# Kernel optimization log

Hardware: AMD Instinct MI355X
Metric: run time of the kernel (lower is better)

Reference implementation:

```python
import jax, jax.numpy as jnp
import numpy as np

B = 65536      # batch
C = 1000       # num_classes
D = 256        # feat_dim


def _l2norm(x, eps=1e-12):
    # matches F.normalize(dim=1): v / max(||v||_2, eps)
    n = jnp.linalg.norm(x, axis=1, keepdims=True)
    return x / jnp.maximum(n, eps)


def setup_inputs() -> dict:
    key = jax.random.key(0)
    k1, k2, k3, k4, k5 = jax.random.split(key, 5)
    bound = 1.0 / np.sqrt(D)
    X = jax.random.normal(k1, (B, D), dtype=jnp.float32)
    labels = jax.random.randint(k2, (B,), 0, C)
    signatures = jax.random.uniform(k3, (C, D), dtype=jnp.float32, minval=-bound, maxval=bound)
    b_means = jax.random.uniform(k4, (1, D), dtype=jnp.float32, minval=-bound, maxval=bound)
    b_covs = jax.random.normal(k5, (D, D), dtype=jnp.float32)
    return {"X": X, "labels": labels, "signatures": signatures,
            "b_means": b_means, "b_covs": b_covs}


def reference(X, labels, signatures, b_means, b_covs):
    # SVD-based whitening of background covariance (tiny DxD)
    cov = b_covs @ b_covs.T
    U, eig, _ = jnp.linalg.svd(cov)
    DU = (eig ** -0.5)[:, None] * U.T              # diag(eig^-1/2) @ U^T, [D, D]
    xHat = _l2norm((X - b_means) @ DU.T)           # [B, D]
    sHat = _l2norm(signatures @ DU.T)              # [C, D]
    ACE_targets = xHat @ sHat.T                    # [B, C] cosine scores
    labels = labels.astype(jnp.int32)
    numerator = jnp.take_along_axis(ACE_targets, labels[:, None], axis=1)[:, 0]
    # denominator = exp(true) + sum(exp(others)) == sum over all classes
    loss = -jnp.mean(numerator - jax.nn.logsumexp(ACE_targets, axis=1))
    return (loss, ACE_targets)
```

## Files before the change

### kernel.cpp

```cpp
#include <hip/hip_runtime.h>
#include <hip/hip_bf16.h>
#include <math.h>

#define D_ 256
#define B_ 65536
#define C_ 1000

typedef _Float16 f16x8 __attribute__((ext_vector_type(8)));
typedef _Float16 f16x4 __attribute__((ext_vector_type(4)));
typedef float f32x4 __attribute__((ext_vector_type(4)));

__global__ void transpose_kernel(const float* __restrict__ in, float* __restrict__ out,
                                 double* __restrict__ acc) {
  __shared__ float t[32][33];
  if (blockIdx.x == 0 && threadIdx.x == 0) *acc = 0.0;
  const int bx = blockIdx.x & 7, by = blockIdx.x >> 3;
  const int lx = threadIdx.x & 31, ly = threadIdx.x >> 5;
#pragma unroll
  for (int s = 0; s < 4; ++s) {
    int r = by * 32 + ly + s * 8;
    t[ly + s * 8][lx] = in[r * 256 + bx * 32 + lx];
  }
  __syncthreads();
#pragma unroll
  for (int s = 0; s < 4; ++s) {
    int r = bx * 32 + ly + s * 8;
    out[r * 256 + by * 32 + lx] = t[lx][ly + s * 8];
  }
}

__global__ void cov_kernel(const float* __restrict__ bc, const float* __restrict__ bcT,
                           double* __restrict__ C64) {
  const int i = blockIdx.x, j = threadIdx.x;
  __shared__ float ri[D_];
  ri[j] = bc[i * D_ + j];
  __syncthreads();
  double s = 0.0;
#pragma unroll 8
  for (int k = 0; k < D_; ++k) s += (double)ri[k] * (double)bcT[k * D_ + j];
  C64[i * D_ + j] = s;
}

__global__ __launch_bounds__(256, 1) void chol_panel(double* __restrict__ A, int p) {
  const int j0 = p * 64;
  const int r = threadIdx.x;
  __shared__ double rowv[64];
  __shared__ double dinv;
  double pr[64];
  const bool act = (r >= j0);
  if (act) {
#pragma unroll
    for (int k = 0; k < 64; ++k) pr[k] = A[(size_t)r * D_ + j0 + k];
  }
#pragma unroll
  for (int j = 0; j < 64; ++j) {
    const int col = j0 + j;
    if (r == col) { double d = sqrt(pr[j]); pr[j] = d; dinv = 1.0 / d; }
    __syncthreads();
    if (r > col) {
      double lr = pr[j] * dinv;
      pr[j] = lr;
      if (r < j0 + 64) rowv[r - j0] = lr;
    }
    __syncthreads();
    if (r > col) {
      const double lr = pr[j];
#pragma unroll
      for (int k = j + 1; k < 64; ++k) pr[k] -= lr * rowv[k];
    }
  }
  if (act) {
    const int kmax = (r - j0 < 63) ? (r - j0) : 63;
#pragma unroll
    for (int k = 0; k < 64; ++k)
      if (k <= kmax) A[(size_t)r * D_ + j0 + k] = pr[k];
  }
}

__global__ __launch_bounds__(256) void chol_trail(double* __restrict__ A, int p) {
  const int j0 = p * 64;
  const int t0 = j0 + 64;
  int b = blockIdx.x, I = 0;
  while (b >= I + 1) { b -= I + 1; ++I; }
  const int J = b;
  const int r0 = t0 + I * 64, c0 = t0 + J * 64;
  __shared__ double LR[64][67];
  __shared__ double LC[64][67];
  const int tid = threadIdx.x;
  for (int e = tid; e < 64 * 64; e += 256) {
    int rr = e >> 6, cc = e & 63;
    LR[rr][cc] = A[(size_t)(r0 + rr) * D_ + j0 + cc];
    LC[rr][cc] = A[(size_t)(c0 + rr) * D_ + j0 + cc];
  }
  __syncthreads();
  const int tx = tid & 15, ty = tid >> 4;
  double acc[4][4];
#pragma unroll
  for (int i = 0; i < 4; ++i)
#pragma unroll
    for (int j = 0; j < 4; ++j) acc[i][j] = 0.0;
#pragma unroll 4
  for (int k = 0; k < 64; ++k) {
    double a_[4], b_[4];
#pragma unroll
    for (int i = 0; i < 4; ++i) a_[i] = LR[ty + 16 * i][k];
#pragma unroll
    for (int j = 0; j < 4; ++j) b_[j] = LC[tx + 16 * j][k];
#pragma unroll
    for (int i = 0; i < 4; ++i)
#pragma unroll
      for (int j = 0; j < 4; ++j) acc[i][j] += a_[i] * b_[j];
  }
#pragma unroll
  for (int i = 0; i < 4; ++i) {
    const int grow = r0 + ty + 16 * i;
#pragma unroll
    for (int j = 0; j < 4; ++j) {
      const int gcol = c0 + tx + 16 * j;
      A[(size_t)grow * D_ + gcol] -= acc[i][j];
    }
  }
}

__global__ __launch_bounds__(256) void inv_kernel(const double* __restrict__ L,
                                                  _Float16* __restrict__ Wb,
                                                  _Float16* __restrict__ WbT) {
  const int c = blockIdx.x;
  const int tid = threadIdx.x;
  __shared__ double w[D_];
  __shared__ double rdi[D_];
  __shared__ double rhs[32];
  __shared__ double Ldd[32][33];
  w[tid] = 0.0;
  rdi[tid] = 1.0 / L[(size_t)tid * D_ + tid];
  __syncthreads();
  const int q0 = c >> 5;
  for (int q = q0; q < 8; ++q) {
    const int i0 = q * 32;
    const int ii = tid >> 3, s = tid & 7;
    const int i = i0 + ii;
    double part = 0.0;
    for (int k = c + s; k < i0; k += 8) part += L[(size_t)i * D_ + k] * w[k];
    part += __shfl_xor(part, 1, 64);
    part += __shfl_xor(part, 2, 64);
    part += __shfl_xor(part, 4, 64);
    if (s == 0) rhs[ii] = ((i == c) ? 1.0 : 0.0) - part;
    for (int e = tid; e < 32 * 32; e += 256) {
      int rr = e >> 5, cc = e & 31;
      Ldd[rr][cc] = L[(size_t)(i0 + rr) * D_ + i0 + cc];
    }
    __syncthreads();
    if (tid < 32) {
      double x = rhs[tid];
      double v = 0.0;
      for (int j = 0; j < 32; ++j) {
        double xj = __shfl(x, j, 64);
        double wj = xj * rdi[i0 + j];
        if (tid == j) v = wj;
        if (tid > j) x -= Ldd[tid][j] * wj;
      }
      w[i0 + tid] = v;
    }
    __syncthreads();
  }
  _Float16 h = (_Float16)(float)w[tid];
  WbT[(size_t)c * D_ + tid] = h;
  Wb[(size_t)tid * D_ + c] = h;
}

__global__ void sig_kernel(const float* __restrict__ S, const _Float16* __restrict__ WbT,
                           _Float16* __restrict__ sHatP) {
  int c = blockIdx.x, i = threadIdx.x;
  const int g = c >> 4, lr = c & 15;
  const int ks = i >> 5, lq = (i >> 3) & 3, jj = i & 7;
  const size_t off = (size_t)(g * 8 + ks) * 512 + (size_t)(lq * 16 + lr) * 8 + jj;
  if (c >= C_) { sHatP[off] = (_Float16)0.0f; return; }
  __shared__ float srow[D_];
  __shared__ float wred[4];
  srow[i] = S[c * D_ + i];
  __syncthreads();
  float t = 0.f;
  for (int k = 0; k < D_; ++k) t += (float)WbT[k * D_ + i] * srow[k];
  float ss = t * t;
#pragma unroll
  for (int d = 1; d < 64; d <<= 1) ss += __shfl_xor(ss, d, 64);
  if ((i & 63) == 0) wred[i >> 6] = ss;
  __syncthreads();
  float tot = wred[0] + wred[1] + wred[2] + wred[3];
  float rn = 1.0f / fmaxf(sqrtf(tot), 1e-12f);
  sHatP[off] = (_Float16)(t * rn);
}

__global__ __launch_bounds__(256) void xform_kernel(const float* __restrict__ X,
                                                    const float* __restrict__ means,
                                                    const _Float16* __restrict__ Wb,
                                                    _Float16* __restrict__ xHat,
                                                    float* __restrict__ rnX) {
  __shared__ __align__(16) _Float16 As[64 * D_];
  __shared__ __align__(16) _Float16 Bs[128 * D_];
  __shared__ float msh[D_];
  const int tid = threadIdx.x;
  const int rowbase = blockIdx.x * 64;
  msh[tid] = means[tid];
  __syncthreads();
  for (int s = 0; s < 16; ++s) {
    int c = s * 256 + tid;
    int r = c >> 6, q = c & 63;
    const float4 xv = *(const float4*)(X + (size_t)(rowbase + r) * D_ + q * 4);
    f16x4 hv;
    hv[0] = (_Float16)(xv.x - msh[q * 4 + 0]);
    hv[1] = (_Float16)(xv.y - msh[q * 4 + 1]);
    hv[2] = (_Float16)(xv.z - msh[q * 4 + 2]);
    hv[3] = (_Float16)(xv.w - msh[q * 4 + 3]);
    int byte = (q * 8) ^ ((r & 7) << 4);
    *(f16x4*)((char*)(As + r * D_) + byte) = hv;
  }
  const int w = tid >> 6, l = tid & 63, lr = l & 15, lq = l >> 4;
  float ss[4] = {0.f, 0.f, 0.f, 0.f};
  for (int ch = 0; ch < 2; ++ch) {
    __syncthreads();
    for (int s = 0; s < 16; ++s) {
      int c = s * 256 + tid;
      int r = c >> 5, q = c & 31;
      uint4 v = *(const uint4*)(Wb + (size_t)(ch * 128 + r) * D_ + q * 8);
      int byte = (q * 16) ^ ((r & 7) << 4);
      *(uint4*)((char*)(Bs + r * D_) + byte) = v;
    }
    __syncthreads();
    f32x4 acc[8];
#pragma unroll
    for (int t = 0; t < 8; ++t) acc[t] = (f32x4){0.f, 0.f, 0.f, 0.f};
#pragma unroll
    for (int ks = 0; ks < 8; ++ks) {
      int arow = w * 16 + lr;
      int abyte = (ks * 64 + lq * 16) ^ ((arow & 7) << 4);
      f16x8 af = *(const f16x8*)((char*)(As + arow * D_) + abyte);
#pragma unroll
      for (int t = 0; t < 8; ++t) {
        int brow = t * 16 + lr;
        int bbyte = (ks * 64 + lq * 16) ^ ((brow & 7) << 4);
        f16x8 bf = *(const f16x8*)((char*)(Bs + brow * D_) + bbyte);
        acc[t] = __builtin_amdgcn_mfma_f32_16x16x32_f16(af, bf, acc[t], 0, 0, 0);
      }
    }
#pragma unroll
    for (int t = 0; t < 8; ++t) {
      int col = ch * 128 + t * 16 + lr;
#pragma unroll
      for (int j = 0; j < 4; ++j) {
        int row = rowbase + w * 16 + lq * 4 + j;
        float v = acc[t][j];
        ss[j] += v * v;
        xHat[(size_t)row * D_ + col] = (_Float16)v;
      }
    }
  }
#pragma unroll
  for (int d = 1; d < 16; d <<= 1) {
#pragma unroll
    for (int j = 0; j < 4; ++j) ss[j] += __shfl_xor(ss[j], d, 64);
  }
  if (lr == 0) {
#pragma unroll
    for (int j = 0; j < 4; ++j) {
      int row = rowbase + w * 16 + lq * 4 + j;
      rnX[row] = 1.0f / fmaxf(sqrtf(ss[j]), 1e-12f);
    }
  }
}

__global__ __launch_bounds__(256) void ace_kernel(const _Float16* __restrict__ xHat,
                                                  const _Float16* __restrict__ sHatP,
                                                  const float* __restrict__ rnX,
                                                  const int* __restrict__ labels,
                                                  float* __restrict__ outACE,
                                                  double* __restrict__ acc_loss) {
  __shared__ float part[16];
  const int tid = threadIdx.x;
  const int w = tid >> 6, l = tid & 63, lr = l & 15, lq = l >> 4;
  const int rowbase = blockIdx.x * 64;
  const int arow = rowbase + w * 16 + lr;

  f16x8 a[8];
  {
    const _Float16* ap = xHat + (size_t)arow * D_ + lq * 8;
#pragma unroll
    for (int ks = 0; ks < 8; ++ks) a[ks] = *(const f16x8*)(ap + ks * 32);
  }

  int lab[4]; float rx[4], ssum[4], num[4];
#pragma unroll
  for (int j = 0; j < 4; ++j) {
    int row = rowbase + w * 16 + lq * 4 + j;
    lab[j] = labels[row];
    rx[j] = rnX[row];
    ssum[j] = 0.f; num[j] = 0.f;
  }

  const _Float16* bl = sHatP + (size_t)l * 8;
  float* const outrow = outACE + (size_t)(rowbase + w * 16 + lq * 4) * C_;

  for (int ch = 0; ch < 8; ++ch) {
    f32x4 acc[8];
#pragma unroll
    for (int t = 0; t < 8; ++t) acc[t] = (f32x4){0.f, 0.f, 0.f, 0.f};
#pragma unroll
    for (int ks = 0; ks < 8; ++ks) {
#pragma unroll
      for (int t = 0; t < 8; ++t) {
        f16x8 bf = *(const f16x8*)(bl + (size_t)((ch * 8 + t) * 8 + ks) * 512);
        acc[t] = __builtin_amdgcn_mfma_f32_16x16x32_f16(a[ks], bf, acc[t], 0, 0, 0);
      }
    }
#pragma unroll
    for (int t = 0; t < 8; ++t) {
      const int col = ch * 128 + t * 16 + lr;
#pragma unroll
      for (int j = 0; j < 4; ++j) {
        float v = acc[t][j] * rx[j];
        if (col < C_) outrow[(size_t)j * C_ + col] = v;
        ssum[j] += __expf(v - 1.0f);
        num[j] = (col == lab[j]) ? v : num[j];
      }
    }
  }
#pragma unroll
  for (int d2 = 1; d2 < 16; d2 <<= 1) {
#pragma unroll
    for (int j = 0; j < 4; ++j) {
      ssum[j] += __shfl_xor(ssum[j], d2, 64);
      num[j]  += __shfl_xor(num[j], d2, 64);
    }
  }
  if (lr == 0) {
    const float padcorr = 24.0f * __expf(-1.0f);
    float contrib = 0.f;
#pragma unroll
    for (int j = 0; j < 4; ++j)
      contrib += num[j] - (1.0f + __logf(ssum[j] - padcorr));
    part[w * 4 + lq] = contrib;
  }
  __syncthreads();
  if (tid == 0) {
    float s = 0.f;
#pragma unroll
    for (int p2 = 0; p2 < 16; ++p2) s += part[p2];
    atomicAdd(acc_loss, (double)s);
  }
}

__global__ void fin_kernel(const double* a, float* out) {
  out[0] = (float)(-(*a) / (double)B_);
}

extern "C" void kernel_launch(void* const* d_in, const int* in_sizes, int n_in,
                              void* d_out, int out_size, void* d_ws, size_t ws_size,
                              hipStream_t stream) {
  const float* X      = (const float*)d_in[0];
  const int*   labels = (const int*)d_in[1];
  const float* S      = (const float*)d_in[2];
  const float* means  = (const float*)d_in[3];
  const float* bc     = (const float*)d_in[4];
  float* out = (float*)d_out;

  char* w = (char*)d_ws;
  double*    acc   = (double*)(w + 0);
  double*    C64   = (double*)(w + 256);
  _Float16*  Wb    = (_Float16*)(w + 524544);
  _Float16*  WbT   = (_Float16*)(w + 655616);
  _Float16*  sHatP = (_Float16*)(w + 786688);
  float*     rnX   = (float*)(w + 1310976);
  _Float16*  xHat  = (_Float16*)(w + 1573120);
  float*     bcT   = (float*)(w + 1573120);

  transpose_kernel<<<64, 256, 0, stream>>>(bc, bcT, acc);
  cov_kernel<<<256, 256, 0, stream>>>(bc, bcT, C64);
  for (int p = 0; p < 4; ++p) {
    chol_panel<<<1, 256, 0, stream>>>(C64, p);
    int nt = 3 - p;
    if (nt > 0) chol_trail<<<nt * (nt + 1) / 2, 256, 0, stream>>>(C64, p);
  }
  inv_kernel<<<256, 256, 0, stream>>>(C64, Wb, WbT);
  sig_kernel<<<1024, 256, 0, stream>>>(S, WbT, sHatP);
  xform_kernel<<<1024, 256, 0, stream>>>(X, means, Wb, xHat, rnX);
  ace_kernel<<<1024, 256, 0, stream>>>(xHat, sHatP, rnX, labels, out + 1, acc);
  fin_kernel<<<1, 1, 0, stream>>>(acc, out);
}
```

Baseline: 446.5 us.

## Stage signature tiles into LDS with double-buffered async loads in ace kernel

The ace kernel now uses 512-thread blocks covering 128 rows and stages each 128-class chunk of the packed signature matrix into shared memory with global_load_lds, double-buffered so the next chunk loads during the current chunk's MFMAs. Before, each wave read B fragments straight from global or L2 memory. The aim is to cut redundant global traffic for the B operand by sharing it across 8 waves and to hide load latency. In exchange it uses 128KB of LDS per block, which caps occupancy at one block per CU, and adds a block barrier per chunk.

```diff
diff --git a/kernel.cpp b/kernel.cpp
--- a/kernel.cpp
+++ b/kernel.cpp
@@ -269,21 +269,22 @@
   }
 }
 
-__global__ __launch_bounds__(256) void ace_kernel(const _Float16* __restrict__ xHat,
+__global__ __launch_bounds__(512) void ace_kernel(const _Float16* __restrict__ xHat,
                                                   const _Float16* __restrict__ sHatP,
                                                   const float* __restrict__ rnX,
                                                   const int* __restrict__ labels,
                                                   float* __restrict__ outACE,
                                                   double* __restrict__ acc_loss) {
-  __shared__ float part[16];
+  __shared__ __align__(16) _Float16 Bsh[2][64 * 512];
+  __shared__ float part[32];
   const int tid = threadIdx.x;
-  const int w = tid >> 6, l = tid & 63, lr = l & 15, lq = l >> 4;
-  const int rowbase = blockIdx.x * 64;
-  const int arow = rowbase + w * 16 + lr;
+  const int wid = tid >> 6, l = tid & 63, lr = l & 15, lq = l >> 4;
+  const int rowbase = blockIdx.x * 128;
+  const int wrow = rowbase + wid * 16;
 
   f16x8 a[8];
   {
-    const _Float16* ap = xHat + (size_t)arow * D_ + lq * 8;
+    const _Float16* ap = xHat + (size_t)(wrow + lr) * D_ + lq * 8;
 #pragma unroll
     for (int ks = 0; ks < 8; ++ks) a[ks] = *(const f16x8*)(ap + ks * 32);
   }
@@ -291,16 +292,31 @@
   int lab[4]; float rx[4], ssum[4], num[4];
 #pragma unroll
   for (int j = 0; j < 4; ++j) {
-    int row = rowbase + w * 16 + lq * 4 + j;
+    int row = wrow + lq * 4 + j;
     lab[j] = labels[row];
     rx[j] = rnX[row];
     ssum[j] = 0.f; num[j] = 0.f;
   }
 
-  const _Float16* bl = sHatP + (size_t)l * 8;
-  float* const outrow = outACE + (size_t)(rowbase + w * 16 + lq * 4) * C_;
-
+#define STAGE(bufi, chi) do {                                                        \
+    const _Float16* _src = sHatP + (size_t)(chi) * 32768;                            \
+    _Float16* _dst = &Bsh[bufi][0];                                                  \
+    _Pragma("unroll")                                                                \
+    for (int _s = 0; _s < 8; ++_s) {                                                 \
+      const int _off = wid * 4096 + _s * 512;                                        \
+      __builtin_amdgcn_global_load_lds(                                              \
+          (const __attribute__((address_space(1))) unsigned int*)(_src + _off + l * 8), \
+          (__attribute__((address_space(3))) unsigned int*)(_dst + _off), 16, 0, 0); \
+    } } while (0)
+
+  float* const outrow = outACE + (size_t)(wrow + lq * 4) * C_;
+
+  STAGE(0, 0);
+  __syncthreads();
+  int buf = 0;
   for (int ch = 0; ch < 8; ++ch) {
+    if (ch < 7) STAGE(buf ^ 1, ch + 1);
+    const _Float16* bb = &Bsh[buf][(size_t)l * 8];
     f32x4 acc[8];
 #pragma unroll
     for (int t = 0; t < 8; ++t) acc[t] = (f32x4){0.f, 0.f, 0.f, 0.f};
@@ -308,22 +324,27 @@
     for (int ks = 0; ks < 8; ++ks) {
 #pragma unroll
       for (int t = 0; t < 8; ++t) {
-        f16x8 bf = *(const f16x8*)(bl + (size_t)((ch * 8 + t) * 8 + ks) * 512);
+        f16x8 bf = *(const f16x8*)(bb + (t * 8 + ks) * 512);
         acc[t] = __builtin_amdgcn_mfma_f32_16x16x32_f16(a[ks], bf, acc[t], 0, 0, 0);
       }
     }
 #pragma unroll
     for (int t = 0; t < 8; ++t) {
       const int col = ch * 128 + t * 16 + lr;
+      const bool valid = (col < C_);
 #pragma unroll
       for (int j = 0; j < 4; ++j) {
         float v = acc[t][j] * rx[j];
-        if (col < C_) outrow[(size_t)j * C_ + col] = v;
+        if (valid) outrow[(size_t)j * C_ + col] = v;
         ssum[j] += __expf(v - 1.0f);
         num[j] = (col == lab[j]) ? v : num[j];
       }
     }
-  }
+    __syncthreads();
+    buf ^= 1;
+  }
+#undef STAGE
+
 #pragma unroll
   for (int d2 = 1; d2 < 16; d2 <<= 1) {
 #pragma unroll
@@ -332,19 +353,21 @@
       num[j]  += __shfl_xor(num[j], d2, 64);
     }
   }
+  if (lr == 0 && lq == 0) {
+  }
   if (lr == 0) {
     const float padcorr = 24.0f * __expf(-1.0f);
     float contrib = 0.f;
 #pragma unroll
     for (int j = 0; j < 4; ++j)
       contrib += num[j] - (1.0f + __logf(ssum[j] - padcorr));
-    part[w * 4 + lq] = contrib;
+    part[wid * 4 + lq] = contrib;
   }
   __syncthreads();
   if (tid == 0) {
     float s = 0.f;
 #pragma unroll
-    for (int p2 = 0; p2 < 16; ++p2) s += part[p2];
+    for (int p2 = 0; p2 < 32; ++p2) s += part[p2];
     atomicAdd(acc_loss, (double)s);
   }
 }
@@ -383,6 +406,6 @@
   inv_kernel<<<256, 256, 0, stream>>>(C64, Wb, WbT);
   sig_kernel<<<1024, 256, 0, stream>>>(S, WbT, sHatP);
   xform_kernel<<<1024, 256, 0, stream>>>(X, means, Wb, xHat, rnX);
-  ace_kernel<<<1024, 256, 0, stream>>>(xHat, sHatP, rnX, labels, out + 1, acc);
+  ace_kernel<<<512, 512, 0, stream>>>(xHat, sHatP, rnX, labels, out + 1, acc);
   fin_kernel<<<1, 1, 0, stream>>>(acc, out);
 }
```

After: 388.3 us. 1.15x faster.
